# Optimization experiments

Measured on AMD Instinct MI355X. Metric: run time of the kernel, lower is better.

Reference implementation:

```python
import jax, jax.numpy as jnp
import numpy as np
import math

B, NB, NA, NC, D, E, H = 4, 2048, 1024, 1024, 1024, 8, 16
HD = D // H
TOP_K = 2
T_MAX = 1000.0
TAU_MIN, TAU_MAX = 0.5, 2.0
W_MIN, W_MAX = 0.1, 0.2
CAP_LO, CAP_HI = 0.5, 0.6
FLOOR = min(0.05, 0.15 / E)       # cfg.routing_floor property
ALPHA = min(FLOOR * E, 1.0)       # routing-floor interpolation weight
BIAS_COEFF = 0.01
EPS = 1e-8


def _layernorm(x, g, b, eps=1e-5):
    mu = x.mean(-1, keepdims=True)
    var = ((x - mu) ** 2).mean(-1, keepdims=True)
    return (x - mu) * jax.lax.rsqrt(var + eps) * g + b


def _forward(tokens_B, output_A, output_C, in_proj_w, in_proj_b, out_proj_w, out_proj_b,
             ln_g, ln_b, te_w1, te_b1, te_w2, te_b2,
             gate_w1, gate_b1, gate_w2, gate_b2, expert_bias, t):
    t_norm = t.astype(jnp.float32) / T_MAX                 # (B,)
    ctx_C = jax.lax.stop_gradient(output_C)                # stopgrad_C_to_B
    ctx_AC = jnp.concatenate([output_A, ctx_C], axis=1)    # (B, NA+NC, D)

    # --- cross attention (torch nn.MultiheadAttention, batch_first) ---
    wq, wk, wv = jnp.split(in_proj_w, 3, axis=0)
    bq, bk, bv = jnp.split(in_proj_b, 3)
    q = (tokens_B @ wq.T + bq).reshape(B, NB, H, HD)
    k = (ctx_AC @ wk.T + bk).reshape(B, NA + NC, H, HD)
    v = (ctx_AC @ wv.T + bv).reshape(B, NA + NC, H, HD)
    scores = jnp.einsum('bqhd,bkhd->bhqk', q, k) / math.sqrt(HD)
    attn = jax.nn.softmax(scores, axis=-1)
    ctx = jnp.einsum('bhqk,bkhd->bqhd', attn, v).reshape(B, NB, D)
    ctx_B = ctx @ out_proj_w.T + out_proj_b
    ctx_B = _layernorm(ctx_B + tokens_B, ln_g, ln_b)

    # --- sinusoidal timestep embedding + 2-layer MLP ---
    half = D // 2
    freq = jnp.exp(-math.log(10000.0) * jnp.arange(half, dtype=jnp.float32) / (half - 1))
    args = t.astype(jnp.float32)[:, None] * freq
    emb = jnp.concatenate([jnp.sin(args), jnp.cos(args)], axis=-1)   # (B, D)
    t_emb = jax.nn.silu(emb @ te_w1.T + te_b1) @ te_w2.T + te_b2     # (B, D)
    t_emb = jnp.broadcast_to(t_emb[:, None, :], (B, NB, D))

    # --- gate MLP + expert bias + temperature ---
    gate_in = jnp.concatenate([tokens_B, ctx_B, t_emb], axis=-1)     # (B, NB, 3D)
    logits = jax.nn.relu(gate_in @ gate_w1.T + gate_b1) @ gate_w2.T + gate_b2 + expert_bias
    tau = (TAU_MIN + (TAU_MAX - TAU_MIN) * t_norm)[:, None, None]
    probs = jax.nn.softmax(logits / tau, axis=-1)                    # (B, NB, E)

    # routing floor: interpolate toward uniform
    probs = (1.0 - ALPHA) * probs + ALPHA / E

    # shared expert injection: expert 0 gets scheduled weight w(t), rest renormalised
    w = (W_MIN + (W_MAX - W_MIN) * t_norm)[:, None, None]
    shared = jnp.maximum(probs[..., 0:1], w)
    others = probs[..., 1:]
    others = others / jnp.maximum(others.sum(-1, keepdims=True), EPS) * (1.0 - shared)
    probs = jnp.concatenate([shared, others], axis=-1)

    # top-k mask (keep top-k probs, zero the rest)
    vals, idx = jax.lax.top_k(probs, TOP_K)
    dispatch = (jax.nn.one_hot(idx, E, dtype=probs.dtype) * vals[..., None]).sum(-2)

    # token-level hard cap (torch.no_grad -> stop_gradient) with redistribution
    cap = (CAP_LO + (CAP_HI - CAP_LO) * t_norm)[:, None, None]
    excess = jax.nn.relu(dispatch - cap)
    capped = dispatch - excess
    headroom = jax.nn.relu(cap - capped)
    head_sum = jnp.maximum(headroom.sum(-1, keepdims=True), EPS)
    capped = capped + excess.sum(-1, keepdims=True) * (headroom / head_sum)
    dispatch = jax.lax.stop_gradient(capped)

    # batch-level utilisation penalty on specialists 1..E-1
    fair = NB / max(E - 1, 1)
    load = dispatch.sum(axis=1).mean(axis=0)                          # (E,)
    pen_excess = jax.nn.relu(load[1:] - fair * 1.5)
    bias_penalty = BIAS_COEFF * jnp.sum(pen_excess ** 2)

    combine = dispatch / (dispatch.sum(-1, keepdims=True) + EPS)
    return dispatch, combine, bias_penalty


def setup_inputs() -> dict:
    key = jax.random.key(0)
    ks = jax.random.split(key, 12)
    g = lambda k, sh: jax.random.normal(k, sh, jnp.float32) * 0.02
    return dict(
        tokens_B=jax.random.normal(ks[0], (B, NB, D), jnp.float32),
        output_A=jax.random.normal(ks[1], (B, NA, D), jnp.float32),
        output_C=jax.random.normal(ks[2], (B, NC, D), jnp.float32),
        t=jax.random.randint(ks[3], (B,), 0, 1000, jnp.int32),
        in_proj_w=g(ks[4], (3 * D, D)),
        in_proj_b=jnp.zeros((3 * D,), jnp.float32),
        out_proj_w=g(ks[5], (D, D)),
        out_proj_b=jnp.zeros((D,), jnp.float32),
        ln_g=jnp.ones((D,), jnp.float32),
        ln_b=jnp.zeros((D,), jnp.float32),
        te_w1=g(ks[6], (2 * D, D)),
        te_b1=jnp.zeros((2 * D,), jnp.float32),
        te_w2=g(ks[7], (D, 2 * D)),
        te_b2=jnp.zeros((D,), jnp.float32),
        gate_w1=g(ks[8], (D, 3 * D)),
        gate_b1=jnp.zeros((D,), jnp.float32),
        gate_w2=g(ks[9], (E, D)),
        gate_b2=jnp.zeros((E,), jnp.float32),
        expert_bias=jnp.zeros((E,), jnp.float32),
    )


def reference(tokens_B, output_A, output_C, t, in_proj_w, in_proj_b, out_proj_w, out_proj_b,
              ln_g, ln_b, te_w1, te_b1, te_w2, te_b2,
              gate_w1, gate_b1, gate_w2, gate_b2, expert_bias):
    return _forward(tokens_B, output_A, output_C, in_proj_w, in_proj_b, out_proj_w, out_proj_b,
                    ln_g, ln_b, te_w1, te_b1, te_w2, te_b2,
                    gate_w1, gate_b1, gate_w2, gate_b2, expert_bias, t)
```

## Files before the change

kernel.cpp:

```cpp
#include <hip/hip_runtime.h>
#include <math.h>


typedef __attribute__((ext_vector_type(8))) short short8;
typedef __attribute__((ext_vector_type(4))) float f32x4;
typedef __attribute__((ext_vector_type(4))) unsigned int u32x4;
typedef unsigned short u16;
typedef unsigned int u32;

__global__ void zero_k(double* p) {
    if (threadIdx.x < 8) p[threadIdx.x] = 0.0;
}

__device__ inline u16 bf_hi(float x) {
    u32 u = __float_as_uint(x);
    u += 0x7FFFu + ((u >> 16) & 1u);
    return (u16)(u >> 16);
}
__device__ inline u16 bf_lo(float x, u16 h) {
    float hf = __uint_as_float(((u32)h) << 16);
    return bf_hi(x - hf);
}
__device__ inline u32 pack_bf(float x) {
    u32 u = __float_as_uint(x);
    u32 hi = (u + (0x7FFFu + ((u >> 16) & 1u))) >> 16;
    float hf = __uint_as_float(hi << 16);
    float d = x - hf;
    u32 u2 = __float_as_uint(d);
    u32 lo = (u2 + (0x7FFFu + ((u2 >> 16) & 1u))) >> 16;
    return (hi << 16) | lo;
}

__device__ inline void pack2(float p0, float p1, u32& o0, u32& o1) {
    u32 h01, l01;
    asm("v_cvt_pk_bf16_f32 %0, %1, %2" : "=v"(h01) : "v"(p0), "v"(p1));
    float d0 = p0 - __uint_as_float(h01 << 16);
    float d1 = p1 - __uint_as_float(h01 & 0xffff0000u);
    asm("v_cvt_pk_bf16_f32 %0, %1, %2" : "=v"(l01) : "v"(d0), "v"(d1));
    o0 = __builtin_amdgcn_perm(h01, l01, 0x05040100u);
    o1 = __builtin_amdgcn_perm(h01, l01, 0x07060302u);
}

__device__ inline void async16(const u16* g, u16* l) {
    __builtin_amdgcn_global_load_lds(
        (const __attribute__((address_space(1))) unsigned int*)g,
        (__attribute__((address_space(3))) unsigned int*)l,
        16, 0, 0);
}

__global__ __launch_bounds__(256)
void split_k(const float* __restrict__ in, u16* __restrict__ hi,
             u16* __restrict__ lo, int n4) {
    int i = blockIdx.x * 256 + threadIdx.x;
    if (i >= n4) return;
    float4 x = ((const float4*)in)[i];
    ushort4 h, l;
    h.x = bf_hi(x.x); l.x = bf_lo(x.x, h.x);
    h.y = bf_hi(x.y); l.y = bf_lo(x.y, h.y);
    h.z = bf_hi(x.z); l.z = bf_lo(x.z, h.z);
    h.w = bf_hi(x.w); l.w = bf_lo(x.w, h.w);
    ((ushort4*)hi)[i] = h;
    ((ushort4*)lo)[i] = l;
}

__global__ void emb_k(const int* __restrict__ t, float* __restrict__ emb) {
    int b = blockIdx.x;
    int j = threadIdx.x;
    float x1 = (float)(-9.210340371976184) * (float)j;
    float x2 = x1 / 511.0f;
    float freq = (float)exp((double)x2);
    float tf = (float)t[b];
    float arg = tf * freq;
    emb[b * 1024 + j]       = (float)sin((double)arg);
    emb[b * 1024 + 512 + j] = (float)cos((double)arg);
}

__global__ void te_fc_k(const float* __restrict__ in, const float* __restrict__ W,
                        const float* __restrict__ bias, float* __restrict__ out,
                        int K, int N, int do_silu) {
    int b = blockIdx.x;
    int wv = threadIdx.x >> 6, lane = threadIdx.x & 63;
    const float* inb = in + (size_t)b * K;
    int n0 = blockIdx.y * 16 + wv * 4;
    for (int q = 0; q < 4; q++) {
        int n = n0 + q;
        const float* wr = W + (size_t)n * K;
        float acc = 0.f;
        for (int c = lane * 4; c < K; c += 256) {
            float4 a  = *(const float4*)(inb + c);
            float4 w4 = *(const float4*)(wr + c);
            acc += a.x * w4.x + a.y * w4.y + a.z * w4.z + a.w * w4.w;
        }
#pragma unroll
        for (int off = 1; off < 64; off <<= 1) acc += __shfl_xor(acc, off, 64);
        if (lane == 0) {
            float x = acc + bias[n];
            out[(size_t)b * N + n] = do_silu ? (x / (1.0f + expf(-x))) : x;
        }
    }
}

template<bool GATE, bool RELU, int OMODE>
__global__ __launch_bounds__(256, 2)
void bfgemm_k(const u16* __restrict__ A0h, const u16* __restrict__ A0l,
              const u16* __restrict__ A1h, const u16* __restrict__ A1l,
              const u16* __restrict__ A2h, const u16* __restrict__ A2l,
              const u16* __restrict__ Wh_g, const u16* __restrict__ Wl_g,
              const float* __restrict__ bias, float* __restrict__ C,
              u16* __restrict__ Chi, u16* __restrict__ Clo, int K, float scale)
{
    __shared__ u16 Ah[128 * 32];
    __shared__ u16 Al[128 * 32];
    __shared__ u16 Wh[128 * 32];
    __shared__ u16 Wl[128 * 32];
    const int tid = threadIdx.x;
    const int row0 = blockIdx.x * 128;
    const int col0 = blockIdx.y * 128;
    const int wv = tid >> 6;
    const int lane = tid & 63;
    const int wrow = (wv & 1) * 64;
    const int wcol = (wv >> 1) * 64;
    const int l15 = lane & 15, quad = lane >> 4;

    f32x4 acc[4][4];
#pragma unroll
    for (int i = 0; i < 4; i++)
#pragma unroll
        for (int j = 0; j < 4; j++)
            acc[i][j] = (f32x4){0.f, 0.f, 0.f, 0.f};

    const int ar0 = tid >> 2, ak0 = (tid & 3) * 8;
    const int ar1 = (tid + 256) >> 2, ak1 = ((tid + 256) & 3) * 8;

    for (int kc = 0; kc < K; kc += 32) {
        const u16* pAh = A0h;
        const u16* pAl = A0l;
        int kk = kc;
        int tembseg = 0;
        if (GATE) {
            int seg = kc >> 10;
            if (seg == 1) { pAh = A1h; pAl = A1l; }
            else if (seg == 2) { pAh = A2h; pAl = A2l; tembseg = 1; }
            kk = kc & 1023;
        }
        const int astr = GATE ? 1024 : K;
        int g0 = row0 + ar0, g1 = row0 + ar1;
        if (GATE && tembseg) { g0 >>= 11; g1 >>= 11; }
        uint4 vah0 = *(const uint4*)&pAh[(size_t)g0 * astr + kk + ak0];
        uint4 vah1 = *(const uint4*)&pAh[(size_t)g1 * astr + kk + ak1];
        uint4 val0 = *(const uint4*)&pAl[(size_t)g0 * astr + kk + ak0];
        uint4 val1 = *(const uint4*)&pAl[(size_t)g1 * astr + kk + ak1];
        uint4 vwh0 = *(const uint4*)&Wh_g[(size_t)(col0 + ar0) * K + kc + ak0];
        uint4 vwh1 = *(const uint4*)&Wh_g[(size_t)(col0 + ar1) * K + kc + ak1];
        uint4 vwl0 = *(const uint4*)&Wl_g[(size_t)(col0 + ar0) * K + kc + ak0];
        uint4 vwl1 = *(const uint4*)&Wl_g[(size_t)(col0 + ar1) * K + kc + ak1];
        __syncthreads();
        *(uint4*)&Ah[ar0 * 32 + ak0] = vah0;
        *(uint4*)&Ah[ar1 * 32 + ak1] = vah1;
        *(uint4*)&Al[ar0 * 32 + ak0] = val0;
        *(uint4*)&Al[ar1 * 32 + ak1] = val1;
        *(uint4*)&Wh[ar0 * 32 + ak0] = vwh0;
        *(uint4*)&Wh[ar1 * 32 + ak1] = vwh1;
        *(uint4*)&Wl[ar0 * 32 + ak0] = vwl0;
        *(uint4*)&Wl[ar1 * 32 + ak1] = vwl1;
        __syncthreads();

        short8 a_h[4], a_l[4];
#pragma unroll
        for (int i = 0; i < 4; i++) {
            int r = (wrow + i * 16 + l15) * 32 + quad * 8;
            a_h[i] = *(const short8*)&Ah[r];
            a_l[i] = *(const short8*)&Al[r];
        }
#pragma unroll
        for (int j = 0; j < 4; j++) {
            int c = (wcol + j * 16 + l15) * 32 + quad * 8;
            short8 b_h = *(const short8*)&Wh[c];
            short8 b_l = *(const short8*)&Wl[c];
#pragma unroll
            for (int i = 0; i < 4; i++) {
                acc[i][j] = __builtin_amdgcn_mfma_f32_16x16x32_bf16(a_h[i], b_h, acc[i][j], 0, 0, 0);
                acc[i][j] = __builtin_amdgcn_mfma_f32_16x16x32_bf16(a_h[i], b_l, acc[i][j], 0, 0, 0);
                acc[i][j] = __builtin_amdgcn_mfma_f32_16x16x32_bf16(a_l[i], b_h, acc[i][j], 0, 0, 0);
            }
        }
    }

#pragma unroll
    for (int i = 0; i < 4; i++) {
#pragma unroll
        for (int j = 0; j < 4; j++) {
            int cc = col0 + wcol + j * 16 + l15;
#pragma unroll
            for (int r = 0; r < 4; r++) {
                int rr = row0 + wrow + i * 16 + quad * 4 + r;
                float v = (acc[i][j][r] + ((OMODE == 3) ? bias[rr] : bias[cc])) * scale;
                if (RELU) v = fmaxf(v, 0.f);
                if (OMODE == 0) {
                    C[(size_t)rr * 1024 + cc] = v;
                } else if (OMODE == 1) {
                    u32 pk = pack_bf(v);
                    size_t a = (size_t)rr * 1024 + cc;
                    Chi[a] = (u16)(pk >> 16); Clo[a] = (u16)pk;
                } else if (OMODE == 2) {
                    int orow = ((rr >> 10) & 3) * 2048 + (rr >> 12) * 1024 + (rr & 1023);
                    u32 pk = pack_bf(v);
                    size_t a = (size_t)orow * 1024 + cc;
                    Chi[a] = (u16)(pk >> 16); Clo[a] = (u16)pk;
                } else {
                    int bb2 = (cc >> 10) & 3;
                    int key = (cc >> 12) * 1024 + (cc & 1023);
                    u32 pk = pack_bf(v);
                    size_t a = ((size_t)(bb2 * 1024 + rr)) * 2048 + key;
                    Chi[a] = (u16)(pk >> 16); Clo[a] = (u16)pk;
                }
            }
        }
    }
}

__global__ __launch_bounds__(512)
void attn_k(const u16* Qh, const u16* Ql,
            const u16* __restrict__ Kh, const u16* __restrict__ Kl,
            const u16* __restrict__ Vh, const u16* __restrict__ Vl,
            u16* Oh, u16* Ol)
{
    __shared__ u32 Pu[256 * 64];
    __shared__ u16 Kb[2][2][64 * 64];
    __shared__ u16 Vb[2][2][64 * 64];

    const int tid = threadIdx.x;
    const int w = tid >> 6, lane = tid & 63;
    const int l15 = lane & 15, quad = lane >> 4;
    const int bh = blockIdx.x, b = bh >> 4, h = bh & 15;
    const int qw = blockIdx.y * 256 + w * 32;
    const int qrow0 = b * 2048 + qw;

    short8 qh_f[2][2], ql_f[2][2];
#pragma unroll
    for (int i = 0; i < 2; i++)
#pragma unroll
        for (int kc = 0; kc < 2; kc++) {
            size_t a = (size_t)(qrow0 + i * 16 + l15) * 1024 + h * 64 + kc * 32 + quad * 8;
            qh_f[i][kc] = *(const short8*)&Qh[a];
            ql_f[i][kc] = *(const short8*)&Ql[a];
        }

    const int srow = tid >> 3;
    const int scsw = ((tid & 7) ^ (srow & 7)) << 3;
    const size_t gk_base = ((size_t)(b * 2048) + srow) * 1024 + h * 64 + scsw;
    const size_t gv_base = ((size_t)((b * 16 + h) * 64 + srow)) * 2048 + scsw;

    f32x4 o[2][4];
#pragma unroll
    for (int i = 0; i < 2; i++)
#pragma unroll
        for (int j = 0; j < 4; j++) o[i][j] = (f32x4){0.f, 0.f, 0.f, 0.f};
    float lsum[2] = {0.f, 0.f};
    float lsv[2][4] = {};

    {
        u16* kd = &Kb[0][0][0] + w * 512;
        u16* vd = &Vb[0][0][0] + w * 512;
        async16(&Kh[gk_base], kd);
        async16(&Kl[gk_base], kd + 4096);
        async16(&Vh[gv_base], vd);
        async16(&Vl[gv_base], vd + 4096);
    }
    __syncthreads();

    for (int kt = 0; kt < 32; kt++) {
        const int cur = kt & 1;
        if (kt < 31) {
            const int nxt = cur ^ 1;
            const size_t gk = gk_base + (size_t)(kt + 1) * 65536;
            const size_t gv = gv_base + (size_t)(kt + 1) * 64;
            u16* kd = &Kb[0][0][0] + nxt * 8192 + w * 512;
            u16* vd = &Vb[0][0][0] + nxt * 8192 + w * 512;
            async16(&Kh[gk], kd);
            async16(&Kl[gk], kd + 4096);
            async16(&Vh[gv], vd);
            async16(&Vl[gv], vd + 4096);
        }
        const u16* Ksh = &Kb[0][0][0] + cur * 8192;
        const u16* Ksl = Ksh + 4096;
        const u16* Vs0 = &Vb[0][0][0] + cur * 8192;
        const u16* Vs1 = Vs0 + 4096;

        f32x4 s[2][4];
#pragma unroll
        for (int i = 0; i < 2; i++)
#pragma unroll
            for (int j = 0; j < 4; j++) s[i][j] = (f32x4){0.f, 0.f, 0.f, 0.f};
#pragma unroll
        for (int j = 0; j < 4; j++) {
            int ka = (j * 16 + l15) * 64 + ((quad ^ (l15 & 7)) << 3);
            short8 kh0 = *(const short8*)&Ksh[ka];
            short8 kh1 = *(const short8*)&Ksh[ka ^ 32];
            short8 kl0 = *(const short8*)&Ksl[ka];
            short8 kl1 = *(const short8*)&Ksl[ka ^ 32];
#pragma unroll
            for (int i = 0; i < 2; i++) {
                s[i][j] = __builtin_amdgcn_mfma_f32_16x16x32_bf16(qh_f[i][0], kh0, s[i][j], 0, 0, 0);
                s[i][j] = __builtin_amdgcn_mfma_f32_16x16x32_bf16(qh_f[i][0], kl0, s[i][j], 0, 0, 0);
                s[i][j] = __builtin_amdgcn_mfma_f32_16x16x32_bf16(ql_f[i][0], kh0, s[i][j], 0, 0, 0);
                s[i][j] = __builtin_amdgcn_mfma_f32_16x16x32_bf16(qh_f[i][1], kh1, s[i][j], 0, 0, 0);
                s[i][j] = __builtin_amdgcn_mfma_f32_16x16x32_bf16(qh_f[i][1], kl1, s[i][j], 0, 0, 0);
                s[i][j] = __builtin_amdgcn_mfma_f32_16x16x32_bf16(ql_f[i][1], kh1, s[i][j], 0, 0, 0);
            }
        }
#pragma unroll
        for (int i = 0; i < 2; i++)
#pragma unroll
            for (int j = 0; j < 4; j++) {
                float p0 = exp2f(s[i][j][0]);
                float p1 = exp2f(s[i][j][1]);
                float p2 = exp2f(s[i][j][2]);
                float p3 = exp2f(s[i][j][3]);
                lsv[i][0] += p0; lsv[i][1] += p1;
                lsv[i][2] += p2; lsv[i][3] += p3;
                u32 o0, o1, o2, o3;
                pack2(p0, p1, o0, o1);
                pack2(p2, p3, o2, o3);
                int rb = w * 32 + i * 16 + quad * 4;
                int cq = (j * 4 + (l15 >> 2)) ^ ((quad & 1) << 2);
                int off = l15 & 3;
                Pu[(rb + 0) * 64 + ((cq ^ 0) << 2) + off] = o0;
                Pu[(rb + 1) * 64 + ((cq ^ 1) << 2) + off] = o1;
                Pu[(rb + 2) * 64 + ((cq ^ 2) << 2) + off] = o2;
                Pu[(rb + 3) * 64 + ((cq ^ 3) << 2) + off] = o3;
            }
#pragma unroll
        for (int kc = 0; kc < 2; kc++) {
            short8 ph[2], pl[2];
#pragma unroll
            for (int i = 0; i < 2; i++) {
                int prow = w * 32 + i * 16 + l15;
                int x = l15 & 7;
                int k0 = kc * 8 + quad * 2;
                const u32* basep = &Pu[prow * 64];
                uint4 u0 = *(const uint4*)&basep[(k0 ^ x) << 2];
                uint4 u1 = *(const uint4*)&basep[((k0 + 1) ^ x) << 2];
                union { short8 s; u32x4 u; } hh, ll;
                hh.u = (u32x4){ __builtin_amdgcn_perm(u0.y, u0.x, 0x07060302u),
                                __builtin_amdgcn_perm(u0.w, u0.z, 0x07060302u),
                                __builtin_amdgcn_perm(u1.y, u1.x, 0x07060302u),
                                __builtin_amdgcn_perm(u1.w, u1.z, 0x07060302u) };
                ll.u = (u32x4){ __builtin_amdgcn_perm(u0.y, u0.x, 0x05040100u),
                                __builtin_amdgcn_perm(u0.w, u0.z, 0x05040100u),
                                __builtin_amdgcn_perm(u1.y, u1.x, 0x05040100u),
                                __builtin_amdgcn_perm(u1.w, u1.z, 0x05040100u) };
                ph[i] = hh.s; pl[i] = ll.s;
            }
#pragma unroll
            for (int jd = 0; jd < 4; jd++) {
                int va = (jd * 16 + l15) * 64 + ((((kc << 2) + quad) ^ (l15 & 7)) << 3);
                short8 vvh = *(const short8*)&Vs0[va];
                short8 vvl = *(const short8*)&Vs1[va];
#pragma unroll
                for (int i = 0; i < 2; i++) {
                    o[i][jd] = __builtin_amdgcn_mfma_f32_16x16x32_bf16(ph[i], vvh, o[i][jd], 0, 0, 0);
                    o[i][jd] = __builtin_amdgcn_mfma_f32_16x16x32_bf16(ph[i], vvl, o[i][jd], 0, 0, 0);
                    o[i][jd] = __builtin_amdgcn_mfma_f32_16x16x32_bf16(pl[i], vvh, o[i][jd], 0, 0, 0);
                }
            }
        }
        __syncthreads();
    }
#pragma unroll
    for (int i = 0; i < 2; i++)
#pragma unroll
        for (int r = 0; r < 4; r++) {
            float s2 = lsv[i][r];
            s2 += __shfl_xor(s2, 1, 64);
            s2 += __shfl_xor(s2, 2, 64);
            s2 += __shfl_xor(s2, 4, 64);
            s2 += __shfl_xor(s2, 8, 64);
            lsv[i][r] = s2;
        }
    (void)lsum;
#pragma unroll
    for (int i = 0; i < 2; i++)
#pragma unroll
        for (int jd = 0; jd < 4; jd++)
#pragma unroll
            for (int r = 0; r < 4; r++) {
                float v = o[i][jd][r] / lsv[i][r];
                u32 pk = pack_bf(v);
                size_t a = (size_t)(qrow0 + i * 16 + quad * 4 + r) * 1024 + h * 64 + jd * 16 + l15;
                Oh[a] = (u16)(pk >> 16);
                Ol[a] = (u16)pk;
            }
}

__global__ __launch_bounds__(256)
void ln_split_k(const float* __restrict__ X, const float* __restrict__ T,
                const float* __restrict__ g, const float* __restrict__ bta,
                u16* __restrict__ chi, u16* __restrict__ clo)
{
    __shared__ float red[8];
    int r = blockIdx.x, tid = threadIdx.x;
    size_t base = (size_t)r * 1024 + tid * 4;
    float4 x  = *(const float4*)(X + base);
    float4 tk = *(const float4*)(T + base);
    x.x += tk.x; x.y += tk.y; x.z += tk.z; x.w += tk.w;
    float s = x.x + x.y + x.z + x.w;
#pragma unroll
    for (int off = 1; off < 64; off <<= 1) s += __shfl_xor(s, off, 64);
    int wv = tid >> 6;
    if ((tid & 63) == 0) red[wv] = s;
    __syncthreads();
    float mu = (red[0] + red[1] + red[2] + red[3]) * (1.0f / 1024.0f);
    float dx0 = x.x - mu, dx1 = x.y - mu, dx2 = x.z - mu, dx3 = x.w - mu;
    float ss = dx0 * dx0 + dx1 * dx1 + dx2 * dx2 + dx3 * dx3;
#pragma unroll
    for (int off = 1; off < 64; off <<= 1) ss += __shfl_xor(ss, off, 64);
    if ((tid & 63) == 0) red[4 + wv] = ss;
    __syncthreads();
    float var = (red[4] + red[5] + red[6] + red[7]) * (1.0f / 1024.0f);
    float inv = 1.0f / sqrtf(var + 1e-5f);
    float4 gg = *(const float4*)(g + tid * 4);
    float4 bb = *(const float4*)(bta + tid * 4);
    float y0 = dx0 * inv * gg.x + bb.x;
    float y1 = dx1 * inv * gg.y + bb.y;
    float y2 = dx2 * inv * gg.z + bb.z;
    float y3 = dx3 * inv * gg.w + bb.w;
    ushort4 h, l;
    h.x = bf_hi(y0); l.x = bf_lo(y0, h.x);
    h.y = bf_hi(y1); l.y = bf_lo(y1, h.y);
    h.z = bf_hi(y2); l.z = bf_lo(y2, h.z);
    h.w = bf_hi(y3); l.w = bf_lo(y3, h.w);
    *(ushort4*)&chi[base] = h;
    *(ushort4*)&clo[base] = l;
}

__global__ __launch_bounds__(256)
void logits_k(const float* __restrict__ Hd, const float* __restrict__ W2,
              const float* __restrict__ b2, const float* __restrict__ eb,
              float* __restrict__ Lg)
{
    int gw = (blockIdx.x * 256 + threadIdx.x) >> 6;
    int lane = threadIdx.x & 63;
    const float* h = Hd + (size_t)gw * 1024;
    float4 hv[4];
#pragma unroll
    for (int j = 0; j < 4; j++) hv[j] = *(const float4*)(h + j * 256 + lane * 4);
    float res[8];
#pragma unroll
    for (int e = 0; e < 8; e++) {
        const float* w = W2 + (size_t)e * 1024;
        float acc = 0.f;
#pragma unroll
        for (int j = 0; j < 4; j++) {
            float4 w4 = *(const float4*)(w + j * 256 + lane * 4);
            acc += hv[j].x * w4.x + hv[j].y * w4.y + hv[j].z * w4.z + hv[j].w * w4.w;
        }
#pragma unroll
        for (int off = 1; off < 64; off <<= 1) acc += __shfl_xor(acc, off, 64);
        res[e] = acc;
    }
    if (lane < 8) {
        float v = res[0];
#pragma unroll
        for (int e = 1; e < 8; e++) v = (lane == e) ? res[e] : v;
        Lg[(size_t)gw * 8 + lane] = v + b2[lane] + eb[lane];
    }
}

__global__ __launch_bounds__(256)
void router_k(const float* __restrict__ Lg, const int* __restrict__ t,
              float* __restrict__ outp, double* __restrict__ loadAcc)
{
    __shared__ double wred[4][8];
    int tid = threadIdx.x;
    int r = blockIdx.x * 256 + tid;
    int b = r >> 11;
    float tn  = (float)t[b] / 1000.0f;
    float tau = 0.5f + 1.5f * tn;
    float p[8];
    float mx = -INFINITY;
#pragma unroll
    for (int e = 0; e < 8; e++) { p[e] = Lg[(size_t)r * 8 + e] / tau; mx = fmaxf(mx, p[e]); }
    float sum = 0.f;
#pragma unroll
    for (int e = 0; e < 8; e++) { p[e] = expf(p[e] - mx); sum += p[e]; }
#pragma unroll
    for (int e = 0; e < 8; e++) p[e] = p[e] / sum;
#pragma unroll
    for (int e = 0; e < 8; e++) p[e] = 0.85f * p[e] + 0.01875f;
    float w = 0.1f + 0.1f * tn;
    float shared_p = fmaxf(p[0], w);
    float osum = 0.f;
#pragma unroll
    for (int e = 1; e < 8; e++) osum += p[e];
    float denom_o = fmaxf(osum, 1e-8f);
    float one_m = 1.0f - shared_p;
    p[0] = shared_p;
#pragma unroll
    for (int e = 1; e < 8; e++) p[e] = (p[e] / denom_o) * one_m;
    int i0 = 0; float v0 = p[0];
#pragma unroll
    for (int e = 1; e < 8; e++) if (p[e] > v0) { v0 = p[e]; i0 = e; }
    int i1 = -1; float v1 = -INFINITY;
#pragma unroll
    for (int e = 0; e < 8; e++) if (e != i0 && p[e] > v1) { v1 = p[e]; i1 = e; }
    float cap = 0.5f + 0.1f * tn;
    float dsp[8], capped[8], hr[8];
    float exsum = 0.f, hsum = 0.f;
#pragma unroll
    for (int e = 0; e < 8; e++) {
        float d = ((e == i0) ? v0 : 0.f) + ((e == i1) ? v1 : 0.f);
        float ex = fmaxf(d - cap, 0.f);
        float c = d - ex;
        float hh = fmaxf(cap - c, 0.f);
        capped[e] = c; hr[e] = hh;
        exsum += ex; hsum += hh;
    }
    float hden = fmaxf(hsum, 1e-8f);
    float dsum = 0.f;
#pragma unroll
    for (int e = 0; e < 8; e++) {
        float d = capped[e] + exsum * (hr[e] / hden);
        dsp[e] = d; dsum += d;
    }
    float cden = dsum + 1e-8f;
#pragma unroll
    for (int e = 0; e < 8; e++) {
        outp[(size_t)r * 8 + e] = dsp[e];
        outp[65536 + (size_t)r * 8 + e] = dsp[e] / cden;
    }
    int lane = tid & 63, wv = tid >> 6;
#pragma unroll
    for (int e = 0; e < 8; e++) {
        double s = (double)dsp[e];
#pragma unroll
        for (int off = 1; off < 64; off <<= 1) s += __shfl_xor(s, off, 64);
        if (lane == 0) wred[wv][e] = s;
    }
    __syncthreads();
    if (tid < 8) {
        double s = wred[0][tid] + wred[1][tid] + wred[2][tid] + wred[3][tid];
        atomicAdd(&loadAcc[tid], s);
    }
}

__global__ void penalty_k(const double* __restrict__ loadAcc, float* __restrict__ outp) {
    if (threadIdx.x == 0) {
        const float thr = (float)(2048.0 / 7.0 * 1.5);
        float pen = 0.f;
#pragma unroll
        for (int e = 1; e < 8; e++) {
            float load = (float)(loadAcc[e] / 4.0);
            float x = fmaxf(load - thr, 0.f);
            pen += x * x;
        }
        outp[131072] = 0.01f * pen;
    }
}

extern "C" void kernel_launch(void* const* d_in, const int* in_sizes, int n_in,
                              void* d_out, int out_size, void* d_ws, size_t ws_size,
                              hipStream_t stream)
{
    const float* tokens = (const float*)d_in[0];
    const float* outA   = (const float*)d_in[1];
    const float* outC   = (const float*)d_in[2];
    const int*   tt     = (const int*)  d_in[3];
    const float* in_w   = (const float*)d_in[4];
    const float* in_b   = (const float*)d_in[5];
    const float* op_w   = (const float*)d_in[6];
    const float* op_b   = (const float*)d_in[7];
    const float* lng    = (const float*)d_in[8];
    const float* lnb    = (const float*)d_in[9];
    const float* te_w1  = (const float*)d_in[10];
    const float* te_b1  = (const float*)d_in[11];
    const float* te_w2  = (const float*)d_in[12];
    const float* te_b2  = (const float*)d_in[13];
    const float* g_w1   = (const float*)d_in[14];
    const float* g_b1   = (const float*)d_in[15];
    const float* g_w2   = (const float*)d_in[16];
    const float* g_b2   = (const float*)d_in[17];
    const float* e_bias = (const float*)d_in[18];
    float* out = (float*)d_out;

    float* ws = (float*)d_ws;
    const size_t NM = (size_t)8192 * 1024;
    float* F0     = ws;
    float* temb   = ws + NM;
    float* embb   = temb + 4096;
    float* hte    = embb + 4096;
    float* logitsb = hte + 8192;
    double* loads = (double*)(logitsb + 65536);

    u16* U = (u16*)(loads + 16);
    u16* Tokh = U;
    u16* Tokl = Tokh + NM;
    u16* ActH = Tokl + NM;
    u16* ActL = ActH + NM;
    u16* Qh   = ActL + NM;
    u16* Ql   = Qh + NM;
    u16* Kh   = Ql + NM;
    u16* Kl   = Kh + NM;
    u16* Vth  = Kl + NM;
    u16* Vtl  = Vth + NM;
    u16* Wsh  = Vtl + NM;
    u16* Wsl  = Wsh + (size_t)3 * 1024 * 1024;
    u16* Tbh  = Wsl + (size_t)3 * 1024 * 1024;
    u16* Tbl  = Tbh + 4096;

    zero_k<<<1, 64, 0, stream>>>(loads);
    emb_k<<<4, 512, 0, stream>>>(tt, embb);
    te_fc_k<<<dim3(4, 128), 256, 0, stream>>>(embb, te_w1, te_b1, hte, 1024, 2048, 1);
    te_fc_k<<<dim3(4, 64),  256, 0, stream>>>(hte,  te_w2, te_b2, temb, 2048, 1024, 0);

    split_k<<<8192, 256, 0, stream>>>(tokens, Tokh, Tokl, 8192 * 1024 / 4);
    split_k<<<3072, 256, 0, stream>>>(in_w, Wsh, Wsl, 3 * 1024 * 1024 / 4);
    split_k<<<4096, 256, 0, stream>>>(outA, ActH, ActL, 4096 * 1024 / 4);
    split_k<<<4096, 256, 0, stream>>>(outC, ActH + (size_t)4096 * 1024,
                                      ActL + (size_t)4096 * 1024, 4096 * 1024 / 4);

    bfgemm_k<false, false, 1><<<dim3(64, 8), 256, 0, stream>>>(
        Tokh, Tokl, nullptr, nullptr, nullptr, nullptr,
        Wsh, Wsl, in_b, nullptr, Qh, Ql, 1024, 0.18033688011112042f);
    bfgemm_k<false, false, 2><<<dim3(64, 8), 256, 0, stream>>>(
        ActH, ActL, nullptr, nullptr, nullptr, nullptr,
        Wsh + (size_t)1024 * 1024, Wsl + (size_t)1024 * 1024,
        in_b + 1024, nullptr, Kh, Kl, 1024, 1.0f);
    bfgemm_k<false, false, 3><<<dim3(8, 64), 256, 0, stream>>>(
        Wsh + (size_t)2048 * 1024, Wsl + (size_t)2048 * 1024,
        nullptr, nullptr, nullptr, nullptr,
        ActH, ActL, in_b + 2048, nullptr, Vth, Vtl, 1024, 1.0f);

    attn_k<<<dim3(64, 8), 512, 0, stream>>>(Qh, Ql, Kh, Kl, Vth, Vtl, Qh, Ql);

    split_k<<<1024, 256, 0, stream>>>(op_w, Wsh, Wsl, 1024 * 1024 / 4);
    bfgemm_k<false, false, 0><<<dim3(64, 8), 256, 0, stream>>>(
        Qh, Ql, nullptr, nullptr, nullptr, nullptr,
        Wsh, Wsl, op_b, F0, nullptr, nullptr, 1024, 1.0f);

    ln_split_k<<<8192, 256, 0, stream>>>(F0, tokens, lng, lnb, Kh, Kl);

    split_k<<<4, 256, 0, stream>>>(temb, Tbh, Tbl, 4096 / 4);
    split_k<<<3072, 256, 0, stream>>>(g_w1, Wsh, Wsl, 3072 * 1024 / 4);
    bfgemm_k<true, true, 0><<<dim3(64, 8), 256, 0, stream>>>(
        Tokh, Tokl, Kh, Kl, Tbh, Tbl,
        Wsh, Wsl, g_b1, F0, nullptr, nullptr, 3072, 1.0f);

    logits_k<<<2048, 256, 0, stream>>>(F0, g_w2, g_b2, e_bias, logitsb);
    router_k<<<32, 256, 0, stream>>>(logitsb, tt, out, loads);
    penalty_k<<<1, 64, 0, stream>>>(loads, out);
}
```

Baseline: 825.6 us.

## Keep attention probabilities in registers via transposed S and 16x16x16 MFMA for PV

The attention kernel now computes S transposed (K as the A operand), so each lane's exp'd scores directly form the B operand of a 16x16x16 bf16 MFMA for P·V. This removes the LDS round trip for P (the 64KB Pu buffer and its permute reads). Shared memory shrinks to K/V double buffers only, and launch bounds request 4 waves per SIMD. The output is staged through LDS so stores are vectorized as 16-byte writes. The trade-off is that it uses more, smaller MFMAs for PV and adds an epilogue transpose.

```diff
diff --git a/kernel.cpp b/kernel.cpp
--- a/kernel.cpp
+++ b/kernel.cpp
@@ -3,6 +3,7 @@
 
 
 typedef __attribute__((ext_vector_type(8))) short short8;
+typedef __attribute__((ext_vector_type(4))) short sh4;
 typedef __attribute__((ext_vector_type(4))) float f32x4;
 typedef __attribute__((ext_vector_type(4))) unsigned int u32x4;
 typedef unsigned short u16;
@@ -39,6 +40,37 @@
     asm("v_cvt_pk_bf16_f32 %0, %1, %2" : "=v"(l01) : "v"(d0), "v"(d1));
     o0 = __builtin_amdgcn_perm(h01, l01, 0x05040100u);
     o1 = __builtin_amdgcn_perm(h01, l01, 0x07060302u);
+}
+
+__device__ inline void pfrag(const f32x4 s, sh4& hi, sh4& lo, float& acc) {
+    float p0 = exp2f(s[0]), p1 = exp2f(s[1]), p2 = exp2f(s[2]), p3 = exp2f(s[3]);
+    acc += (p0 + p1) + (p2 + p3);
+    u32 h01, h23, l01, l23;
+    asm("v_cvt_pk_bf16_f32 %0, %1, %2" : "=v"(h01) : "v"(p0), "v"(p1));
+    asm("v_cvt_pk_bf16_f32 %0, %1, %2" : "=v"(h23) : "v"(p2), "v"(p3));
+    float d0 = p0 - __uint_as_float(h01 << 16);
+    float d1 = p1 - __uint_as_float(h01 & 0xffff0000u);
+    float d2 = p2 - __uint_as_float(h23 << 16);
+    float d3 = p3 - __uint_as_float(h23 & 0xffff0000u);
+    asm("v_cvt_pk_bf16_f32 %0, %1, %2" : "=v"(l01) : "v"(d0), "v"(d1));
+    asm("v_cvt_pk_bf16_f32 %0, %1, %2" : "=v"(l23) : "v"(d2), "v"(d3));
+    union { u32 u[2]; sh4 s4; } H, L;
+    H.u[0] = h01; H.u[1] = h23;
+    L.u[0] = l01; L.u[1] = l23;
+    hi = H.s4; lo = L.s4;
+}
+
+__device__ inline f32x4 mfma32(short8 a, short8 b, f32x4 c) {
+    return __builtin_amdgcn_mfma_f32_16x16x32_bf16(a, b, c, 0, 0, 0);
+}
+__device__ inline f32x4 mfma16(sh4 a, sh4 b, f32x4 c) {
+#if __has_builtin(__builtin_amdgcn_mfma_f32_16x16x16bf16_1k)
+    return __builtin_amdgcn_mfma_f32_16x16x16bf16_1k(a, b, c, 0, 0, 0);
+#else
+    asm volatile("v_mfma_f32_16x16x16_bf16 %0, %1, %2, %0"
+                 : "+v"(c) : "v"(a), "v"(b));
+    return c;
+#endif
 }
 
 __device__ inline void async16(const u16* g, u16* l) {
@@ -219,15 +251,15 @@
     }
 }
 
-__global__ __launch_bounds__(512)
+__global__ __launch_bounds__(512, 4)
 void attn_k(const u16* Qh, const u16* Ql,
             const u16* __restrict__ Kh, const u16* __restrict__ Kl,
             const u16* __restrict__ Vh, const u16* __restrict__ Vl,
             u16* Oh, u16* Ol)
 {
-    __shared__ u32 Pu[256 * 64];
-    __shared__ u16 Kb[2][2][64 * 64];
-    __shared__ u16 Vb[2][2][64 * 64];
+    __shared__ __align__(16) u16 smem[32768];
+    u16* Kbase = smem;
+    u16* Vbase = smem + 16384;
 
     const int tid = threadIdx.x;
     const int w = tid >> 6, lane = tid & 63;
@@ -251,17 +283,16 @@
     const size_t gk_base = ((size_t)(b * 2048) + srow) * 1024 + h * 64 + scsw;
     const size_t gv_base = ((size_t)((b * 16 + h) * 64 + srow)) * 2048 + scsw;
 
-    f32x4 o[2][4];
-#pragma unroll
-    for (int i = 0; i < 2; i++)
-#pragma unroll
-        for (int j = 0; j < 4; j++) o[i][j] = (f32x4){0.f, 0.f, 0.f, 0.f};
+    f32x4 o[4][2];
+#pragma unroll
+    for (int dt = 0; dt < 4; dt++)
+#pragma unroll
+        for (int i = 0; i < 2; i++) o[dt][i] = (f32x4){0.f, 0.f, 0.f, 0.f};
     float lsum[2] = {0.f, 0.f};
-    float lsv[2][4] = {};
 
     {
-        u16* kd = &Kb[0][0][0] + w * 512;
-        u16* vd = &Vb[0][0][0] + w * 512;
+        u16* kd = Kbase + w * 512;
+        u16* vd = Vbase + w * 512;
         async16(&Kh[gk_base], kd);
         async16(&Kl[gk_base], kd + 4096);
         async16(&Vh[gv_base], vd);
@@ -275,122 +306,108 @@
             const int nxt = cur ^ 1;
             const size_t gk = gk_base + (size_t)(kt + 1) * 65536;
             const size_t gv = gv_base + (size_t)(kt + 1) * 64;
-            u16* kd = &Kb[0][0][0] + nxt * 8192 + w * 512;
-            u16* vd = &Vb[0][0][0] + nxt * 8192 + w * 512;
+            u16* kd = Kbase + nxt * 8192 + w * 512;
+            u16* vd = Vbase + nxt * 8192 + w * 512;
             async16(&Kh[gk], kd);
             async16(&Kl[gk], kd + 4096);
             async16(&Vh[gv], vd);
             async16(&Vl[gv], vd + 4096);
         }
-        const u16* Ksh = &Kb[0][0][0] + cur * 8192;
+        const u16* Ksh = Kbase + cur * 8192;
         const u16* Ksl = Ksh + 4096;
-        const u16* Vs0 = &Vb[0][0][0] + cur * 8192;
-        const u16* Vs1 = Vs0 + 4096;
-
-        f32x4 s[2][4];
-#pragma unroll
-        for (int i = 0; i < 2; i++)
-#pragma unroll
-            for (int j = 0; j < 4; j++) s[i][j] = (f32x4){0.f, 0.f, 0.f, 0.f};
-#pragma unroll
-        for (int j = 0; j < 4; j++) {
-            int ka = (j * 16 + l15) * 64 + ((quad ^ (l15 & 7)) << 3);
+        const u16* Vsh = Vbase + cur * 8192;
+        const u16* Vsl = Vsh + 4096;
+
+#pragma unroll
+        for (int jt = 0; jt < 4; jt++) {
+            f32x4 st0 = (f32x4){0.f, 0.f, 0.f, 0.f};
+            f32x4 st1 = (f32x4){0.f, 0.f, 0.f, 0.f};
+            const int ka = (jt * 16 + l15) * 64 + ((quad ^ (l15 & 7)) << 3);
             short8 kh0 = *(const short8*)&Ksh[ka];
             short8 kh1 = *(const short8*)&Ksh[ka ^ 32];
             short8 kl0 = *(const short8*)&Ksl[ka];
             short8 kl1 = *(const short8*)&Ksl[ka ^ 32];
-#pragma unroll
-            for (int i = 0; i < 2; i++) {
-                s[i][j] = __builtin_amdgcn_mfma_f32_16x16x32_bf16(qh_f[i][0], kh0, s[i][j], 0, 0, 0);
-                s[i][j] = __builtin_amdgcn_mfma_f32_16x16x32_bf16(qh_f[i][0], kl0, s[i][j], 0, 0, 0);
-                s[i][j] = __builtin_amdgcn_mfma_f32_16x16x32_bf16(ql_f[i][0], kh0, s[i][j], 0, 0, 0);
-                s[i][j] = __builtin_amdgcn_mfma_f32_16x16x32_bf16(qh_f[i][1], kh1, s[i][j], 0, 0, 0);
-                s[i][j] = __builtin_amdgcn_mfma_f32_16x16x32_bf16(qh_f[i][1], kl1, s[i][j], 0, 0, 0);
-                s[i][j] = __builtin_amdgcn_mfma_f32_16x16x32_bf16(ql_f[i][1], kh1, s[i][j], 0, 0, 0);
+            st0 = mfma32(kh0, qh_f[0][0], st0);
+            st0 = mfma32(kl0, qh_f[0][0], st0);
+            st0 = mfma32(kh0, ql_f[0][0], st0);
+            st0 = mfma32(kh1, qh_f[0][1], st0);
+            st0 = mfma32(kl1, qh_f[0][1], st0);
+            st0 = mfma32(kh1, ql_f[0][1], st0);
+            st1 = mfma32(kh0, qh_f[1][0], st1);
+            st1 = mfma32(kl0, qh_f[1][0], st1);
+            st1 = mfma32(kh0, ql_f[1][0], st1);
+            st1 = mfma32(kh1, qh_f[1][1], st1);
+            st1 = mfma32(kl1, qh_f[1][1], st1);
+            st1 = mfma32(kh1, ql_f[1][1], st1);
+            sh4 phi0, plo0, phi1, plo1;
+            pfrag(st0, phi0, plo0, lsum[0]);
+            pfrag(st1, phi1, plo1, lsum[1]);
+#pragma unroll
+            for (int dt = 0; dt < 4; dt++) {
+                const int va = (dt * 16 + l15) * 64
+                             + (((jt * 2 + (quad >> 1)) ^ (l15 & 7)) << 3)
+                             + (quad & 1) * 4;
+                sh4 vvh = *(const sh4*)&Vsh[va];
+                sh4 vvl = *(const sh4*)&Vsl[va];
+                o[dt][0] = mfma16(vvh, phi0, o[dt][0]);
+                o[dt][0] = mfma16(vvl, phi0, o[dt][0]);
+                o[dt][0] = mfma16(vvh, plo0, o[dt][0]);
+                o[dt][1] = mfma16(vvh, phi1, o[dt][1]);
+                o[dt][1] = mfma16(vvl, phi1, o[dt][1]);
+                o[dt][1] = mfma16(vvh, plo1, o[dt][1]);
             }
         }
-#pragma unroll
-        for (int i = 0; i < 2; i++)
-#pragma unroll
-            for (int j = 0; j < 4; j++) {
-                float p0 = exp2f(s[i][j][0]);
-                float p1 = exp2f(s[i][j][1]);
-                float p2 = exp2f(s[i][j][2]);
-                float p3 = exp2f(s[i][j][3]);
-                lsv[i][0] += p0; lsv[i][1] += p1;
-                lsv[i][2] += p2; lsv[i][3] += p3;
-                u32 o0, o1, o2, o3;
-                pack2(p0, p1, o0, o1);
-                pack2(p2, p3, o2, o3);
-                int rb = w * 32 + i * 16 + quad * 4;
-                int cq = (j * 4 + (l15 >> 2)) ^ ((quad & 1) << 2);
-                int off = l15 & 3;
-                Pu[(rb + 0) * 64 + ((cq ^ 0) << 2) + off] = o0;
-                Pu[(rb + 1) * 64 + ((cq ^ 1) << 2) + off] = o1;
-                Pu[(rb + 2) * 64 + ((cq ^ 2) << 2) + off] = o2;
-                Pu[(rb + 3) * 64 + ((cq ^ 3) << 2) + off] = o3;
+        __syncthreads();
+    }
+
+#pragma unroll
+    for (int i = 0; i < 2; i++) {
+        float s2 = lsum[i];
+        s2 += __shfl_xor(s2, 16, 64);
+        s2 += __shfl_xor(s2, 32, 64);
+        lsum[i] = 1.0f / s2;
+    }
+
+    u32* otr = (u32*)smem + w * 2048;
+#pragma unroll
+    for (int i = 0; i < 2; i++) {
+        const int q = i * 16 + l15;
+        const int xm = (q & 7) << 2;
+#pragma unroll
+        for (int dt = 0; dt < 4; dt++) {
+#pragma unroll
+            for (int r = 0; r < 4; r += 2) {
+                float v0 = o[dt][i][r]     * lsum[i];
+                float v1 = o[dt][i][r + 1] * lsum[i];
+                u32 a0, a1;
+                pack2(v0, v1, a0, a1);
+                const int d = dt * 16 + quad * 4 + r;
+                uint2 val; val.x = a0; val.y = a1;
+                *(uint2*)&otr[q * 64 + (d ^ xm)] = val;
             }
-#pragma unroll
-        for (int kc = 0; kc < 2; kc++) {
-            short8 ph[2], pl[2];
-#pragma unroll
-            for (int i = 0; i < 2; i++) {
-                int prow = w * 32 + i * 16 + l15;
-                int x = l15 & 7;
-                int k0 = kc * 8 + quad * 2;
-                const u32* basep = &Pu[prow * 64];
-                uint4 u0 = *(const uint4*)&basep[(k0 ^ x) << 2];
-                uint4 u1 = *(const uint4*)&basep[((k0 + 1) ^ x) << 2];
-                union { short8 s; u32x4 u; } hh, ll;
-                hh.u = (u32x4){ __builtin_amdgcn_perm(u0.y, u0.x, 0x07060302u),
-                                __builtin_amdgcn_perm(u0.w, u0.z, 0x07060302u),
-                                __builtin_amdgcn_perm(u1.y, u1.x, 0x07060302u),
-                                __builtin_amdgcn_perm(u1.w, u1.z, 0x07060302u) };
-                ll.u = (u32x4){ __builtin_amdgcn_perm(u0.y, u0.x, 0x05040100u),
-                                __builtin_amdgcn_perm(u0.w, u0.z, 0x05040100u),
-                                __builtin_amdgcn_perm(u1.y, u1.x, 0x05040100u),
-                                __builtin_amdgcn_perm(u1.w, u1.z, 0x05040100u) };
-                ph[i] = hh.s; pl[i] = ll.s;
-            }
-#pragma unroll
-            for (int jd = 0; jd < 4; jd++) {
-                int va = (jd * 16 + l15) * 64 + ((((kc << 2) + quad) ^ (l15 & 7)) << 3);
-                short8 vvh = *(const short8*)&Vs0[va];
-                short8 vvl = *(const short8*)&Vs1[va];
-#pragma unroll
-                for (int i = 0; i < 2; i++) {
-                    o[i][jd] = __builtin_amdgcn_mfma_f32_16x16x32_bf16(ph[i], vvh, o[i][jd], 0, 0, 0);
-                    o[i][jd] = __builtin_amdgcn_mfma_f32_16x16x32_bf16(ph[i], vvl, o[i][jd], 0, 0, 0);
-                    o[i][jd] = __builtin_amdgcn_mfma_f32_16x16x32_bf16(pl[i], vvh, o[i][jd], 0, 0, 0);
-                }
-            }
-        }
-        __syncthreads();
-    }
-#pragma unroll
-    for (int i = 0; i < 2; i++)
-#pragma unroll
-        for (int r = 0; r < 4; r++) {
-            float s2 = lsv[i][r];
-            s2 += __shfl_xor(s2, 1, 64);
-            s2 += __shfl_xor(s2, 2, 64);
-            s2 += __shfl_xor(s2, 4, 64);
-            s2 += __shfl_xor(s2, 8, 64);
-            lsv[i][r] = s2;
-        }
-    (void)lsum;
-#pragma unroll
-    for (int i = 0; i < 2; i++)
-#pragma unroll
-        for (int jd = 0; jd < 4; jd++)
-#pragma unroll
-            for (int r = 0; r < 4; r++) {
-                float v = o[i][jd][r] / lsv[i][r];
-                u32 pk = pack_bf(v);
-                size_t a = (size_t)(qrow0 + i * 16 + quad * 4 + r) * 1024 + h * 64 + jd * 16 + l15;
-                Oh[a] = (u16)(pk >> 16);
-                Ol[a] = (u16)pk;
-            }
+        }
+    }
+    const int qr = lane >> 1;
+    const int dh = lane & 1;
+    const size_t gq = (size_t)(qrow0 + qr) * 1024 + h * 64 + dh * 32;
+#pragma unroll
+    for (int g = 0; g < 4; g++) {
+        const int c0 = dh * 8 + g * 2;
+        const int m = qr & 7;
+        uint4 x = *(const uint4*)&otr[qr * 64 + ((c0 ^ m) << 2)];
+        uint4 y = *(const uint4*)&otr[qr * 64 + (((c0 + 1) ^ m) << 2)];
+        union { short8 s; u32x4 u; } hh, ll;
+        hh.u = (u32x4){ __builtin_amdgcn_perm(x.y, x.x, 0x07060302u),
+                        __builtin_amdgcn_perm(x.w, x.z, 0x07060302u),
+                        __builtin_amdgcn_perm(y.y, y.x, 0x07060302u),
+                        __builtin_amdgcn_perm(y.w, y.z, 0x07060302u) };
+        ll.u = (u32x4){ __builtin_amdgcn_perm(x.y, x.x, 0x05040100u),
+                        __builtin_amdgcn_perm(x.w, x.z, 0x05040100u),
+                        __builtin_amdgcn_perm(y.y, y.x, 0x05040100u),
+                        __builtin_amdgcn_perm(y.w, y.z, 0x05040100u) };
+        *(short8*)&Oh[gq + g * 8] = hh.s;
+        *(short8*)&Ol[gq + g * 8] = ll.s;
+    }
 }
 
 __global__ __launch_bounds__(256)
```

After: 834.1 us, median of 2. About the same (+1.0%).
